# Optimization experiments

Hardware: AMD Instinct MI355X
Metric: run time of the kernel (lower is better)

The kernel has to match this reference:

```python
import jax, jax.numpy as jnp
import numpy as np
import math

B, C, H, W = 16, 512, 32, 32
HEADS = 8
HD = C // HEADS            # 64 head_dim
NFREQ = HD // 4            # 16 (head_dim % 4 == 0)
MAX_FREQ = 128.0
T = H * W                  # 1024 tokens


def _make_so2_mat():
    # make_2dcoord: meshgrid('ij') of arange(H), arange(W) -> [H, W, 2]
    xg, yg = np.meshgrid(np.arange(H, dtype=np.float32), np.arange(W, dtype=np.float32), indexing='ij')
    coord = np.stack([xg, yg], -1)                                   # [H, W, 2]
    freqs = np.exp(np.linspace(0.0, math.log(MAX_FREQ), NFREQ)).astype(np.float32)  # [NFREQ]
    th = coord[..., None, :] * freqs[None, None, :, None]            # [H, W, NFREQ, 2]
    c, s = np.cos(th), np.sin(th)
    # rotation matrices [[c, -s], [s, c]] -> [H, W, NFREQ, 2(dim), 2, 2]
    mat = np.stack([np.stack([c, -s], -1), np.stack([s, c], -1)], -2)
    mat = mat.reshape(H * W, NFREQ * 2, 2, 2)                        # flatten(2,3) then flatten(0,1)
    return jnp.asarray(mat[:, : HD // 2])                            # [T, HD//2, 2, 2]


def setup_inputs() -> dict:
    key = jax.random.key(0)
    ks = jax.random.split(key, 5)
    mat = _make_so2_mat()
    return {
        'x': jax.random.normal(ks[0], (B, C, H, W), dtype=jnp.float32),
        'w_qkv': jax.random.normal(ks[1], (3 * C, C), dtype=jnp.float32) * 0.02,
        'b_qkv': jax.random.normal(ks[2], (3 * C,), dtype=jnp.float32) * 0.02,
        'w_o': jax.random.normal(ks[3], (C, C), dtype=jnp.float32) * 0.02,
        'b_o': jax.random.normal(ks[4], (C,), dtype=jnp.float32) * 0.02,
        'mat_q': mat,
        'mat_k': mat,
        'mat_v': mat,
        'mat_o': jnp.swapaxes(mat, -2, -1),
    }


def _rep_mul(rep, t):
    # rep: [T, HD//2, 2, 2]; t: [B, nh, T, HD] -> per-pair 2x2 rotation
    tb = t.reshape(B, HEADS, T, HD // 2, 2)
    return jnp.einsum('tfij,bntfj->bntfi', rep, tb).reshape(B, HEADS, T, HD)


def _split_heads(t):
    # 'b (c nh) h w -> b nh (h w) c' (c outer, nh inner in channel dim)
    return t.reshape(B, HD, HEADS, T).transpose(0, 2, 3, 1)


def reference(x, w_qkv, b_qkv, w_o, b_o, mat_q, mat_k, mat_v, mat_o):
    # 1x1 conv QKV projection == channel GEMM
    qkv = jnp.einsum('bchw,oc->bohw', x, w_qkv) + b_qkv[None, :, None, None]
    q, k, v = jnp.split(qkv, 3, axis=1)
    q, k, v = map(_split_heads, (q, k, v))                 # [B, nh, T, HD]
    q = _rep_mul(mat_q, q)
    k = _rep_mul(mat_k, k)
    v = _rep_mul(mat_v, v)
    scale = 1.0 / math.sqrt(HD)
    attn = jax.nn.softmax(jnp.einsum('bntd,bnsd->bnts', q, k) * scale, axis=-1)
    o = jnp.einsum('bnts,bnsd->bntd', attn, v)             # [B, nh, T, HD]
    o = _rep_mul(mat_o, o)
    # 'b nh (h w) c -> b (c nh) h w'
    o = o.reshape(B, HEADS, H, W, HD).transpose(0, 4, 1, 2, 3).reshape(B, C, H, W)
    return jnp.einsum('bchw,oc->bohw', o, w_o) + b_o[None, :, None, None]
```

## Files before the change

kernel.cpp:

```cpp
#include <hip/hip_runtime.h>


typedef __bf16 bf16x8 __attribute__((ext_vector_type(8)));
typedef __bf16 bf16x4 __attribute__((ext_vector_type(4)));
typedef float  f32x4  __attribute__((ext_vector_type(4)));

__device__ __forceinline__ f32x4 mfma16(bf16x8 a, bf16x8 b, f32x4 c) {
    return __builtin_amdgcn_mfma_f32_16x16x32_bf16(a, b, c, 0, 0, 0);
}

__device__ __forceinline__ void async16(const void* g, void* l) {
    __builtin_amdgcn_global_load_lds(
        (const __attribute__((address_space(1))) void*)g,
        (__attribute__((address_space(3))) void*)l, 16, 0, 0);
}

__global__ void k_convert_w(const float* __restrict__ wq, const float* __restrict__ wo,
                            __bf16* __restrict__ wqb, __bf16* __restrict__ wob) {
    int i = blockIdx.x * 256 + threadIdx.x;
    if (i < 3 * 512 * 512) wqb[i] = (__bf16)wq[i];
    if (i < 512 * 512) {
        int o = i >> 9, k2 = i & 511;
        int nh = k2 >> 6, hd = k2 & 63;
        wob[i] = (__bf16)wo[o * 512 + hd * 8 + nh];
    }
}

__global__ void k_transpose_x(const float* __restrict__ x, __bf16* __restrict__ xt) {
    __shared__ float tile[32][33];
    const int b  = blockIdx.z;
    const int c0 = blockIdx.y * 32;
    const int t0 = blockIdx.x * 32;
    const int tx = threadIdx.x, ty = threadIdx.y;
    const float* xp = x + ((size_t)b * 512 + c0) * 1024 + t0;
#pragma unroll
    for (int j = 0; j < 4; j++)
        tile[ty + j * 8][tx] = xp[(ty + j * 8) * 1024 + tx];
    __syncthreads();
    __bf16* xo = xt + ((size_t)b * 1024 + t0) * 512 + c0;
#pragma unroll
    for (int j = 0; j < 4; j++)
        xo[(ty + j * 8) * 512 + tx] = (__bf16)tile[tx][ty + j * 8];
}

__global__ __launch_bounds__(256) void k_gemm_qkv(
        const __bf16* __restrict__ A, const __bf16* __restrict__ W,
        const float* __restrict__ bias,
        const float* __restrict__ matq, const float* __restrict__ matk,
        const float* __restrict__ matv,
        __bf16* __restrict__ qd, __bf16* __restrict__ kd, __bf16* __restrict__ vtd)
{
    __shared__ __bf16 As[128][64];
    __shared__ __bf16 Bs[128][64];
    const int tid = threadIdx.x;
    const int m0 = blockIdx.x * 128;
    const int jb = blockIdx.y;
    const int part = jb >> 2;
    const int nh_base = (jb & 3) * 2;
    const int lane = tid & 63, w = tid >> 6;
    const int ln = lane & 15, quad = lane >> 4;
    const int wr = w >> 1, wc = w & 1;

    const int srow = lane >> 3;
    const int scol = (((lane & 7) ^ srow) * 8);

    const __bf16* arow[4];
    const __bf16* brow[4];
#pragma unroll
    for (int jj = 0; jj < 4; jj++) {
        int rr = w * 32 + jj * 8 + srow;
        arow[jj] = &A[(size_t)(m0 + rr) * 512 + scol];
        int o = part * 512 + (rr & 63) * 8 + nh_base + (rr >> 6);
        brow[jj] = &W[(size_t)o * 512 + scol];
    }

    f32x4 acc[4][4] = {};

    for (int k0 = 0; k0 < 512; k0 += 64) {
#pragma unroll
        for (int jj = 0; jj < 4; jj++)
            async16(arow[jj] + k0, &As[w * 32 + jj * 8][0]);
#pragma unroll
        for (int jj = 0; jj < 4; jj++)
            async16(brow[jj] + k0, &Bs[w * 32 + jj * 8][0]);
        __syncthreads();
#pragma unroll
        for (int h = 0; h < 2; h++) {
            bf16x8 af[4], wf[4];
#pragma unroll
            for (int mi = 0; mi < 4; mi++)
                af[mi] = *(const bf16x8*)&As[wr * 64 + mi * 16 + ln][(((h * 4 + quad) ^ (ln & 7)) * 8)];
#pragma unroll
            for (int ni = 0; ni < 4; ni++)
                wf[ni] = *(const bf16x8*)&Bs[wc * 64 + ni * 16 + ln][(((h * 4 + quad) ^ (ln & 7)) * 8)];
#pragma unroll
            for (int mi = 0; mi < 4; mi++)
#pragma unroll
                for (int ni = 0; ni < 4; ni++)
                    acc[mi][ni] = mfma16(af[mi], wf[ni], acc[mi][ni]);
        }
        __syncthreads();
    }

    const int nh = nh_base + wc;
    const int rowbase = m0 + wr * 64;
    const int b  = rowbase >> 10, t0 = rowbase & 1023;
    const int bh = b * 8 + nh;
    const int ip = ln & 1;
    const float2* matp = (const float2*)(part == 0 ? matq : (part == 1 ? matk : matv));
    __bf16* qkdst = (part == 0) ? qd : kd;
    const float qscale = (part == 0) ? 0.18033688011112042f : 1.0f;

#pragma unroll
    for (int ni = 0; ni < 4; ni++) {
        const int hd = ni * 16 + ln;
        const int f  = hd >> 1;
        const float bias_o = bias[part * 512 + hd * 8 + nh];
#pragma unroll
        for (int mi = 0; mi < 4; mi++) {
            const int tq = t0 + mi * 16 + quad * 4;
            if (part < 2) {
#pragma unroll
                for (int r = 0; r < 4; r++) {
                    int t = tq + r;
                    float val = acc[mi][ni][r] + bias_o;
                    float pr  = __shfl_xor(val, 1);
                    float2 mv = matp[((size_t)t * 32 + f) * 2 + ip];
                    float e  = ip ? pr : val;
                    float oo = ip ? val : pr;
                    float rv = (mv.x * e + mv.y * oo) * qscale;
                    qkdst[((size_t)bh * 1024 + t) * 64 + hd] = (__bf16)rv;
                }
            } else {
                __bf16 pack[4];
#pragma unroll
                for (int r = 0; r < 4; r++) {
                    int t = tq + r;
                    float val = acc[mi][ni][r] + bias_o;
                    float pr  = __shfl_xor(val, 1);
                    float2 mv = matp[((size_t)t * 32 + f) * 2 + ip];
                    float e  = ip ? pr : val;
                    float oo = ip ? val : pr;
                    pack[r] = (__bf16)(mv.x * e + mv.y * oo);
                }
                *(uint2*)&vtd[((size_t)bh * 64 + hd) * 1024 + tq] = *(const uint2*)pack;
            }
        }
    }
}

__global__ __launch_bounds__(512) void k_attn(
        const __bf16* __restrict__ q, const __bf16* __restrict__ kk,
        const __bf16* __restrict__ vt, const float* __restrict__ mato,
        __bf16* __restrict__ od)
{
    __shared__ __bf16 Ks[64][64];
    __shared__ __bf16 Vs[64][64];
    __shared__ __bf16 Ps[8][16][64];
    const int bh = blockIdx.x, qt = blockIdx.y;
    const int tid = threadIdx.x, w = tid >> 6, lane = tid & 63;
    const int ln = lane & 15, quad = lane >> 4;
    const int lx = ln & 7;
    const int srow = lane >> 3;
    const int scol = ((lane & 7) ^ srow) * 8;
    const int qr0 = qt * 128 + w * 16;

    bf16x8 qa[2];
#pragma unroll
    for (int ki = 0; ki < 2; ki++)
        qa[ki] = *(const bf16x8*)&q[((size_t)bh * 1024 + qr0 + ln) * 64 + ki * 32 + quad * 8];

    const __bf16* kbase = kk + (size_t)bh * 1024 * 64;
    const __bf16* vbase = vt + (size_t)bh * 64 * 1024;

    f32x4 oacc[4] = {};
    f32x4 lacc = {};

    bf16x8 ones;
#pragma unroll
    for (int j = 0; j < 8; j++) ones[j] = (__bf16)1.0f;

    for (int st = 0; st < 16; st++) {
        async16(kbase + (size_t)(st * 64 + w * 8 + srow) * 64 + scol, &Ks[w * 8][0]);
        async16(vbase + (size_t)(w * 8 + srow) * 1024 + st * 64 + scol, &Vs[w * 8][0]);
        __syncthreads();

#pragma unroll
        for (int si = 0; si < 4; si++) {
            bf16x8 kb0 = *(const bf16x8*)&Ks[si * 16 + ln][((quad    ) ^ lx) * 8];
            bf16x8 kb1 = *(const bf16x8*)&Ks[si * 16 + ln][((quad + 4) ^ lx) * 8];
            f32x4 sc = {};
            sc = mfma16(kb0, qa[0], sc);
            sc = mfma16(kb1, qa[1], sc);
            bf16x4 pk;
#pragma unroll
            for (int r = 0; r < 4; r++)
                pk[r] = (__bf16)exp2f(sc[r]);
            *(bf16x4*)((char*)&Ps[w][ln][0]
                       + (((si * 2 + (quad >> 1)) ^ lx) * 16) + (quad & 1) * 8) = pk;
        }

#pragma unroll
        for (int kt = 0; kt < 2; kt++) {
            bf16x8 pa = *(const bf16x8*)&Ps[w][ln][((kt * 4 + quad) ^ lx) * 8];
#pragma unroll
            for (int ni = 0; ni < 4; ni++) {
                bf16x8 vb = *(const bf16x8*)&Vs[ni * 16 + ln][((kt * 4 + quad) ^ lx) * 8];
                oacc[ni] = mfma16(vb, pa, oacc[ni]);
            }
            lacc = mfma16(ones, pa, lacc);
        }
        __syncthreads();
    }

    const float invl = 1.0f / lacc[0];
    const float4* mo4 = (const float4*)mato;
    const int t = qr0 + ln;
#pragma unroll
    for (int ni = 0; ni < 4; ni++) {
        const int hd0 = ni * 16 + quad * 4;
        const int f   = hd0 >> 1;
        float v0 = oacc[ni][0] * invl;
        float v1 = oacc[ni][1] * invl;
        float v2 = oacc[ni][2] * invl;
        float v3 = oacc[ni][3] * invl;
        float4 m1 = mo4[(size_t)t * 32 + f];
        float4 m2 = mo4[(size_t)t * 32 + f + 1];
        __bf16 pk[4];
        pk[0] = (__bf16)(m1.x * v0 + m1.y * v1);
        pk[1] = (__bf16)(m1.z * v0 + m1.w * v1);
        pk[2] = (__bf16)(m2.x * v2 + m2.y * v3);
        pk[3] = (__bf16)(m2.z * v2 + m2.w * v3);
        *(uint2*)&od[((size_t)bh * 1024 + t) * 64 + hd0] = *(const uint2*)pk;
    }
}

__global__ __launch_bounds__(256) void k_gemm_out(
        const __bf16* __restrict__ A, const __bf16* __restrict__ W,
        const float* __restrict__ bias, float* __restrict__ out)
{
    __shared__ __bf16 As[128][64];
    __shared__ __bf16 Bs[128][64];
    const int tid = threadIdx.x;
    const int m0 = blockIdx.x * 128;
    const int n0 = blockIdx.y * 128;
    const int lane = tid & 63, w = tid >> 6;
    const int ln = lane & 15, quad = lane >> 4;
    const int wr = w >> 1, wc = w & 1;

    const int srow = lane >> 3;
    const int scol = (((lane & 7) ^ srow) * 8);

    const int bb = m0 >> 10, t00 = m0 & 1023;

    const __bf16* arow[4];
    const __bf16* brow[4];
#pragma unroll
    for (int jj = 0; jj < 4; jj++) {
        int rr = w * 32 + jj * 8 + srow;
        arow[jj] = &A[((size_t)bb * 8192 + t00 + rr) * 64 + scol];
        brow[jj] = &W[(size_t)(n0 + rr) * 512 + scol];
    }

    f32x4 acc[4][4] = {};

    for (int k0 = 0; k0 < 512; k0 += 64) {
#pragma unroll
        for (int jj = 0; jj < 4; jj++)
            async16(arow[jj] + (size_t)k0 * 1024, &As[w * 32 + jj * 8][0]);
#pragma unroll
        for (int jj = 0; jj < 4; jj++)
            async16(brow[jj] + k0, &Bs[w * 32 + jj * 8][0]);
        __syncthreads();
#pragma unroll
        for (int h = 0; h < 2; h++) {
            bf16x8 af[4], wf[4];
#pragma unroll
            for (int mi = 0; mi < 4; mi++)
                af[mi] = *(const bf16x8*)&As[wr * 64 + mi * 16 + ln][(((h * 4 + quad) ^ (ln & 7)) * 8)];
#pragma unroll
            for (int ni = 0; ni < 4; ni++)
                wf[ni] = *(const bf16x8*)&Bs[wc * 64 + ni * 16 + ln][(((h * 4 + quad) ^ (ln & 7)) * 8)];
#pragma unroll
            for (int mi = 0; mi < 4; mi++)
#pragma unroll
                for (int ni = 0; ni < 4; ni++)
                    acc[mi][ni] = mfma16(af[mi], wf[ni], acc[mi][ni]);
        }
        __syncthreads();
    }

    const int rowbase = m0 + wr * 64;
    const int bb2 = rowbase >> 10, t0 = rowbase & 1023;
#pragma unroll
    for (int ni = 0; ni < 4; ni++) {
        int o = n0 + wc * 64 + ni * 16 + ln;
        float bias_o = bias[o];
#pragma unroll
        for (int mi = 0; mi < 4; mi++) {
            int t = t0 + mi * 16 + quad * 4;
            f32x4 v = acc[mi][ni];
            v[0] += bias_o; v[1] += bias_o; v[2] += bias_o; v[3] += bias_o;
            *(f32x4*)&out[((size_t)bb2 * 512 + o) * 1024 + t] = v;
        }
    }
}

extern "C" void kernel_launch(void* const* d_in, const int* in_sizes, int n_in,
                              void* d_out, int out_size, void* d_ws, size_t ws_size,
                              hipStream_t stream) {
    (void)in_sizes; (void)n_in; (void)out_size; (void)ws_size;
    const float* x     = (const float*)d_in[0];
    const float* w_qkv = (const float*)d_in[1];
    const float* b_qkv = (const float*)d_in[2];
    const float* w_o   = (const float*)d_in[3];
    const float* b_o   = (const float*)d_in[4];
    const float* mat_q = (const float*)d_in[5];
    const float* mat_k = (const float*)d_in[6];
    const float* mat_v = (const float*)d_in[7];
    const float* mat_o = (const float*)d_in[8];
    float* out = (float*)d_out;

    char* p = (char*)d_ws;
    __bf16* wqb = (__bf16*)p;  p += (size_t)3 * 512 * 512 * 2;
    __bf16* wob = (__bf16*)p;  p += (size_t)512 * 512 * 2;
    char* xt_base = p;
    __bf16* xt  = (__bf16*)p;  p += (size_t)16384 * 512 * 2;
    __bf16* qd  = (__bf16*)p;  p += (size_t)128 * 1024 * 64 * 2;
    __bf16* kd  = (__bf16*)p;  p += (size_t)128 * 1024 * 64 * 2;
    __bf16* vtd = (__bf16*)p;  p += (size_t)128 * 64 * 1024 * 2;
    __bf16* od  = (__bf16*)xt_base;

    k_convert_w  <<<dim3(3072),       dim3(256),    0, stream>>>(w_qkv, w_o, wqb, wob);
    k_transpose_x<<<dim3(32, 16, 16), dim3(32, 8),  0, stream>>>(x, xt);
    k_gemm_qkv   <<<dim3(128, 12),    dim3(256),    0, stream>>>(xt, wqb, b_qkv, mat_q, mat_k, mat_v, qd, kd, vtd);
    k_attn       <<<dim3(128, 8),     dim3(512),    0, stream>>>(qd, kd, vtd, mat_o, od);
    k_gemm_out   <<<dim3(128, 4),     dim3(256),    0, stream>>>(od, wob, b_o, out);
}
```

Measured before the change: 226.7 us.

## Double-buffer LDS tiles in projection GEMMs and enlarge transpose tile

Both the QKV and output projection GEMMs now use two LDS buffers, issuing the async global-to-LDS loads for the next K-slice before computing on the current one, so memory latency can overlap with MFMA work. The x transpose kernel moves from 32x32 tiles to 64x64 tiles with a 64x4 thread block, giving longer contiguous row accesses and fewer blocks. The cost is double the LDS footprint in the GEMMs, which may reduce occupancy. Whether the trailing barrier still covers the buffer-reuse hazard cannot be checked because that part of the loop is hidden.

```diff
diff --git a/kernel.cpp b/kernel.cpp
--- a/kernel.cpp
+++ b/kernel.cpp
@@ -27,20 +27,20 @@
 }
 
 __global__ void k_transpose_x(const float* __restrict__ x, __bf16* __restrict__ xt) {
-    __shared__ float tile[32][33];
+    __shared__ float tile[64][65];
     const int b  = blockIdx.z;
-    const int c0 = blockIdx.y * 32;
-    const int t0 = blockIdx.x * 32;
+    const int c0 = blockIdx.y * 64;
+    const int t0 = blockIdx.x * 64;
     const int tx = threadIdx.x, ty = threadIdx.y;
     const float* xp = x + ((size_t)b * 512 + c0) * 1024 + t0;
 #pragma unroll
-    for (int j = 0; j < 4; j++)
-        tile[ty + j * 8][tx] = xp[(ty + j * 8) * 1024 + tx];
+    for (int j = 0; j < 16; j++)
+        tile[ty + j * 4][tx] = xp[(ty + j * 4) * 1024 + tx];
     __syncthreads();
     __bf16* xo = xt + ((size_t)b * 1024 + t0) * 512 + c0;
 #pragma unroll
-    for (int j = 0; j < 4; j++)
-        xo[(ty + j * 8) * 512 + tx] = (__bf16)tile[tx][ty + j * 8];
+    for (int j = 0; j < 16; j++)
+        xo[(ty + j * 4) * 512 + tx] = (__bf16)tile[tx][ty + j * 4];
 }
 
 __global__ __launch_bounds__(256) void k_gemm_qkv(
@@ -50,8 +50,8 @@
         const float* __restrict__ matv,
         __bf16* __restrict__ qd, __bf16* __restrict__ kd, __bf16* __restrict__ vtd)
 {
-    __shared__ __bf16 As[128][64];
-    __shared__ __bf16 Bs[128][64];
+    __shared__ __bf16 As[2][128][64];
+    __shared__ __bf16 Bs[2][128][64];
     const int tid = threadIdx.x;
     const int m0 = blockIdx.x * 128;
     const int jb = blockIdx.y;
@@ -76,23 +76,33 @@
 
     f32x4 acc[4][4] = {};
 
-    for (int k0 = 0; k0 < 512; k0 += 64) {
-#pragma unroll
-        for (int jj = 0; jj < 4; jj++)
-            async16(arow[jj] + k0, &As[w * 32 + jj * 8][0]);
-#pragma unroll
-        for (int jj = 0; jj < 4; jj++)
-            async16(brow[jj] + k0, &Bs[w * 32 + jj * 8][0]);
-        __syncthreads();
+#pragma unroll
+    for (int jj = 0; jj < 4; jj++) {
+        async16(arow[jj], &As[0][w * 32 + jj * 8][0]);
+        async16(brow[jj], &Bs[0][w * 32 + jj * 8][0]);
+    }
+    __syncthreads();
+
+#pragma unroll
+    for (int it = 0; it < 8; ++it) {
+        const int cur = it & 1;
+        if (it < 7) {
+            const int k1 = (it + 1) * 64;
+#pragma unroll
+            for (int jj = 0; jj < 4; jj++) {
+                async16(arow[jj] + k1, &As[cur ^ 1][w * 32 + jj * 8][0]);
+                async16(brow[jj] + k1, &Bs[cur ^ 1][w * 32 + jj * 8][0]);
+            }
+        }
 #pragma unroll
         for (int h = 0; h < 2; h++) {
             bf16x8 af[4], wf[4];
 #pragma unroll
             for (int mi = 0; mi < 4; mi++)
-                af[mi] = *(const bf16x8*)&As[wr * 64 + mi * 16 + ln][(((h * 4 + quad) ^ (ln & 7)) * 8)];
+                af[mi] = *(const bf16x8*)&As[cur][wr * 64 + mi * 16 + ln][(((h * 4 + quad) ^ (ln & 7)) * 8)];
 #pragma unroll
             for (int ni = 0; ni < 4; ni++)
-                wf[ni] = *(const bf16x8*)&Bs[wc * 64 + ni * 16 + ln][(((h * 4 + quad) ^ (ln & 7)) * 8)];
+                wf[ni] = *(const bf16x8*)&Bs[cur][wc * 64 + ni * 16 + ln][(((h * 4 + quad) ^ (ln & 7)) * 8)];
 #pragma unroll
             for (int mi = 0; mi < 4; mi++)
 #pragma unroll
@@ -239,8 +249,8 @@
         const __bf16* __restrict__ A, const __bf16* __restrict__ W,
         const float* __restrict__ bias, float* __restrict__ out)
 {
-    __shared__ __bf16 As[128][64];
-    __shared__ __bf16 Bs[128][64];
+    __shared__ __bf16 As[2][128][64];
+    __shared__ __bf16 Bs[2][128][64];
     const int tid = threadIdx.x;
     const int m0 = blockIdx.x * 128;
     const int n0 = blockIdx.y * 128;
@@ -264,23 +274,33 @@
 
     f32x4 acc[4][4] = {};
 
-    for (int k0 = 0; k0 < 512; k0 += 64) {
-#pragma unroll
-        for (int jj = 0; jj < 4; jj++)
-            async16(arow[jj] + (size_t)k0 * 1024, &As[w * 32 + jj * 8][0]);
-#pragma unroll
-        for (int jj = 0; jj < 4; jj++)
-            async16(brow[jj] + k0, &Bs[w * 32 + jj * 8][0]);
-        __syncthreads();
+#pragma unroll
+    for (int jj = 0; jj < 4; jj++) {
+        async16(arow[jj], &As[0][w * 32 + jj * 8][0]);
+        async16(brow[jj], &Bs[0][w * 32 + jj * 8][0]);
+    }
+    __syncthreads();
+
+#pragma unroll
+    for (int it = 0; it < 8; ++it) {
+        const int cur = it & 1;
+        if (it < 7) {
+            const int k1 = (it + 1) * 64;
+#pragma unroll
+            for (int jj = 0; jj < 4; jj++) {
+                async16(arow[jj] + (size_t)k1 * 1024, &As[cur ^ 1][w * 32 + jj * 8][0]);
+                async16(brow[jj] + k1,                &Bs[cur ^ 1][w * 32 + jj * 8][0]);
+            }
+        }
 #pragma unroll
         for (int h = 0; h < 2; h++) {
             bf16x8 af[4], wf[4];
 #pragma unroll
             for (int mi = 0; mi < 4; mi++)
-                af[mi] = *(const bf16x8*)&As[wr * 64 + mi * 16 + ln][(((h * 4 + quad) ^ (ln & 7)) * 8)];
+                af[mi] = *(const bf16x8*)&As[cur][wr * 64 + mi * 16 + ln][(((h * 4 + quad) ^ (ln & 7)) * 8)];
 #pragma unroll
             for (int ni = 0; ni < 4; ni++)
-                wf[ni] = *(const bf16x8*)&Bs[wc * 64 + ni * 16 + ln][(((h * 4 + quad) ^ (ln & 7)) * 8)];
+                wf[ni] = *(const bf16x8*)&Bs[cur][wc * 64 + ni * 16 + ln][(((h * 4 + quad) ^ (ln & 7)) * 8)];
 #pragma unroll
             for (int mi = 0; mi < 4; mi++)
 #pragma unroll
@@ -332,7 +352,7 @@
     __bf16* od  = (__bf16*)xt_base;
 
     k_convert_w  <<<dim3(3072),       dim3(256),    0, stream>>>(w_qkv, w_o, wqb, wob);
-    k_transpose_x<<<dim3(32, 16, 16), dim3(32, 8),  0, stream>>>(x, xt);
+    k_transpose_x<<<dim3(16, 8, 16),  dim3(64, 4),  0, stream>>>(x, xt);
     k_gemm_qkv   <<<dim3(128, 12),    dim3(256),    0, stream>>>(xt, wqb, b_qkv, mat_q, mat_k, mat_v, qd, kd, vtd);
     k_attn       <<<dim3(128, 8),     dim3(512),    0, stream>>>(qd, kd, vtd, mat_o, od);
     k_gemm_out   <<<dim3(128, 4),     dim3(256),    0, stream>>>(od, wob, b_o, out);
```

Result: no change. 229.5 us (+1.2%).
